# Kernel optimization log

Hardware: AMD Instinct MI355X
Metric: run time of the kernel (lower is better)

## Reference

```python
import jax, jax.numpy as jnp
import numpy as np

B, N1, N2 = 8, 16384, 2048
C1, C2 = 128, 256
IN_CH = C1 + C2  # 384
MLP = [256, 128]
BN_EPS = 1e-5


def setup_inputs() -> dict:
    key = jax.random.key(0)
    ks = jax.random.split(key, 12)
    inp = {
        "xyz1": jax.random.normal(ks[0], (B, N1, 3), dtype=jnp.float32),
        "xyz2": jax.random.normal(ks[1], (B, N2, 3), dtype=jnp.float32),
        "points1": jax.random.normal(ks[2], (B, N1, C1), dtype=jnp.float32),
        "points2": jax.random.normal(ks[3], (B, N2, C2), dtype=jnp.float32),
        # pointwise conv1d (kernel=1) weights as [out, in]
        "W1": jax.random.normal(ks[4], (MLP[0], IN_CH), dtype=jnp.float32) * (1.0 / np.sqrt(IN_CH)),
        "b1": jnp.zeros((MLP[0],), dtype=jnp.float32),
        "gamma1": jnp.ones((MLP[0],), dtype=jnp.float32),
        "beta1": jnp.zeros((MLP[0],), dtype=jnp.float32),
        "W2": jax.random.normal(ks[5], (MLP[1], MLP[0]), dtype=jnp.float32) * (1.0 / np.sqrt(MLP[0])),
        "b2": jnp.zeros((MLP[1],), dtype=jnp.float32),
        "gamma2": jnp.ones((MLP[1],), dtype=jnp.float32),
        "beta2": jnp.zeros((MLP[1],), dtype=jnp.float32),
    }
    return inp


def _bn_relu(h, gamma, beta):
    # BatchNorm1d in training mode: batch stats over (B, N) per channel
    mean = jnp.mean(h, axis=(0, 1), keepdims=True)
    var = jnp.mean((h - mean) ** 2, axis=(0, 1), keepdims=True)
    return jax.nn.relu((h - mean) * jax.lax.rsqrt(var + BN_EPS) * gamma + beta)


def reference(xyz1, xyz2, points1, points2, W1, b1, gamma1, beta1, W2, b2, gamma2, beta2):
    # squared pairwise distances [B, N1, N2]
    d = (-2.0 * jnp.einsum("bnc,bmc->bnm", xyz1, xyz2)
         + jnp.sum(xyz1 ** 2, -1)[:, :, None]
         + jnp.sum(xyz2 ** 2, -1)[:, None, :])
    neg_vals, idx = jax.lax.top_k(-d, 3)            # 3 smallest distances
    dists = jnp.maximum(-neg_vals, 1e-10)           # clamp(min=1e-10)
    w = 1.0 / dists                                 # [B, N1, 3]
    w_norm = w / jnp.maximum(jnp.sum(w, axis=2, keepdims=True), 1e-8)
    # gather 3 neighbor features: [B, N1, 3, C2]
    gathered = jax.vmap(lambda p, i: p[i])(points2, idx)
    interp = jnp.einsum("bnk,bnkc->bnc", w_norm, gathered)  # [B, N1, C2]
    x = jnp.concatenate([points1, interp], axis=-1)          # [B, N1, IN_CH]
    # pointwise conv + BN + ReLU stack
    h = jnp.einsum("bnc,oc->bno", x, W1) + b1
    h = _bn_relu(h, gamma1, beta1)
    h = jnp.einsum("bnc,oc->bno", h, W2) + b2
    h = _bn_relu(h, gamma2, beta2)
    return h  # [B, N1, MLP[-1]]
```

## Files before the change

### kernel.cpp

```cpp
#include <hip/hip_runtime.h>
#include <hip/hip_bf16.h>
#include <stdint.h>
#include <stddef.h>

typedef __hip_bfloat16 bf16;
typedef __attribute__((ext_vector_type(8))) short short8;
typedef __attribute__((ext_vector_type(4))) float f32x4;

#define B_SZ   8
#define N1_SZ  16384
#define N2_SZ  2048
#define C1_SZ  128
#define C2_SZ  256
#define IN_CH  384
#define O1_SZ  256
#define O2_SZ  128
#define R_TOT  (B_SZ * N1_SZ)

#define OFF_FLAG   ((size_t)0)
#define OFF_STATS1 ((size_t)256)
#define OFF_SCALE1 ((size_t)2304)
#define OFF_STATS2 ((size_t)4352)
#define OFF_SCALE2 ((size_t)5376)
#define OFF_WIDX   ((size_t)8192)
#define OFF_WW     ((size_t)1581056)
#define OFF_H1     ((size_t)3153920)
#define WS_NEEDED  ((size_t)70262784)


static __device__ __forceinline__ float cvtf(bf16 v) { return __bfloat162float(v); }
static __device__ __forceinline__ float cvtf(float v) { return v; }
static __device__ __forceinline__ bf16  f2b(float v) { return __float2bfloat16(v); }

static __device__ __forceinline__ void load8f(const bf16* p, float* f) {
  uint4 v = *(const uint4*)p;
  const bf16* e = (const bf16*)&v;
#pragma unroll
  for (int j = 0; j < 8; ++j) f[j] = cvtf(e[j]);
}
static __device__ __forceinline__ void load8f(const float* p, float* f) {
  float4 a = *(const float4*)p;
  float4 b = *(const float4*)(p + 4);
  f[0] = a.x; f[1] = a.y; f[2] = a.z; f[3] = a.w;
  f[4] = b.x; f[5] = b.y; f[6] = b.z; f[7] = b.w;
}
static __device__ __forceinline__ void load8b(const bf16* p, bf16* o) {
  *(uint4*)o = *(const uint4*)p;
}
static __device__ __forceinline__ void load8b(const float* p, bf16* o) {
  float f[8]; load8f(p, f);
#pragma unroll
  for (int j = 0; j < 8; ++j) o[j] = f2b(f[j]);
}
static __device__ __forceinline__ void stv(bf16* p, float v) { *p = f2b(v); }
static __device__ __forceinline__ void stv(float* p, float v) { *p = v; }
static __device__ __forceinline__ void store8(bf16* p, const bf16* t) { *(uint4*)p = *(const uint4*)t; }
static __device__ __forceinline__ void store8(float* p, const float* t) {
  *(uint4*)p = *(const uint4*)t; *(uint4*)(p + 4) = *(const uint4*)(t + 4);
}

__global__ void k_detect(const uint16_t* __restrict__ probe, int* __restrict__ flag) {
  __shared__ int cnt;
  if (threadIdx.x == 0) cnt = 0;
  __syncthreads();
  unsigned u = probe[threadIdx.x];
  int e = (u >> 7) & 0xFF;
  if (e >= 100 && e <= 141) atomicAdd(&cnt, 1);
  __syncthreads();
  if (threadIdx.x == 0) *flag = (cnt >= 224) ? 1 : 0;
}

template <typename T>
__global__ __launch_bounds__(256) void k_fill2(T* __restrict__ out,
                                               const int* __restrict__ flag, int expect) {
  if (flag && *flag != expect) return;
  size_t e0 = ((size_t)blockIdx.x * 256 + threadIdx.x) * 8;
  T t[8];
#pragma unroll
  for (int j = 0; j < 8; ++j) stv(&t[j], 2.0f);
  store8(out + e0, t);
}

static __device__ __forceinline__ void merge3(double& a0, double& a1, double& a2,
                                              int& x0, int& x1, int& x2, int mask) {
  double b0 = __shfl_xor(a0, mask, 64);
  double b1 = __shfl_xor(a1, mask, 64);
  double b2 = __shfl_xor(a2, mask, 64);
  int y0 = __shfl_xor(x0, mask, 64);
  int y1 = __shfl_xor(x1, mask, 64);
  int y2 = __shfl_xor(x2, mask, 64);
  bool t = (a0 < b0) || (a0 == b0 && x0 < y0);
  double c0 = t ? a0 : b0; int k0 = t ? x0 : y0;
  double A0 = t ? a1 : a0; int X0 = t ? x1 : x0;
  double A1 = t ? a2 : a1; int X1 = t ? x2 : x1;
  double B0 = t ? b0 : b1; int Y0 = t ? y0 : y1;
  double B1 = t ? b1 : b2; int Y1 = t ? y1 : y2;
  t = (A0 < B0) || (A0 == B0 && X0 < Y0);
  double c1 = t ? A0 : B0; int k1 = t ? X0 : Y0;
  double A0b = t ? A1 : A0; int X0b = t ? X1 : X0;
  double B0b = t ? B0 : B1; int Y0b = t ? Y0 : Y1;
  t = (A0b < B0b) || (A0b == B0b && X0b < Y0b);
  double c2 = t ? A0b : B0b; int k2 = t ? X0b : Y0b;
  a0 = c0; a1 = c1; a2 = c2; x0 = k0; x1 = k1; x2 = k2;
}

template <typename T>
__global__ __launch_bounds__(512) void k_top3(const T* __restrict__ xyz1,
                                              const T* __restrict__ xyz2,
                                              int* __restrict__ widx,
                                              float* __restrict__ ww,
                                              const int* __restrict__ flag, int expect) {
  if (*flag != expect) return;
  __shared__ float4 sp[N2_SZ];
  int b = blockIdx.x >> 7;
  int g = blockIdx.x & 127;
  const T* x2 = xyz2 + (size_t)b * N2_SZ * 3;
  for (int i = threadIdx.x; i < N2_SZ; i += 512) {
    float px = cvtf(x2[i * 3 + 0]);
    float py = cvtf(x2[i * 3 + 1]);
    float pz = cvtf(x2[i * 3 + 2]);
    double dx = (double)px, dy = (double)py, dz = (double)pz;
    float pw = (float)(dx * dx + dy * dy + dz * dz);
    sp[i] = make_float4(-2.f * px, -2.f * py, -2.f * pz, pw);
  }
  __syncthreads();
  int qloc = threadIdx.x >> 2;
  int sub  = threadIdx.x & 3;
  int n = g * 128 + qloc;
  int r = b * N1_SZ + n;
  float Qxf = cvtf(xyz1[(size_t)r * 3 + 0]);
  float Qyf = cvtf(xyz1[(size_t)r * 3 + 1]);
  float Qzf = cvtf(xyz1[(size_t)r * 3 + 2]);

  float m0 = 3.0e38f, m1 = 3.0e38f, m2 = 3.0e38f, m3 = 3.0e38f;
  int i0 = 0, i1 = 0, i2 = 0, i3 = 0;
#pragma unroll 4
  for (int i = 0; i < N2_SZ / 4; ++i) {
    int j = (i << 2) | sub;
    float4 p = sp[j];
    float d = fmaf(p.x, Qxf, fmaf(p.y, Qyf, fmaf(p.z, Qzf, p.w)));
    bool c0 = d < m0, c1 = d < m1, c2 = d < m2, c3 = d < m3;
    int t3 = c2 ? i2 : (c3 ? j : i3);
    int t2 = c1 ? i1 : (c2 ? j : i2);
    int t1 = c0 ? i0 : (c1 ? j : i1);
    int t0 = c0 ? j : i0;
    float v3 = __builtin_amdgcn_fmed3f(m2, m3, d);
    float v2 = __builtin_amdgcn_fmed3f(m1, m2, d);
    float v1 = __builtin_amdgcn_fmed3f(m0, m1, d);
    float v0 = fminf(m0, d);
    m0 = v0; m1 = v1; m2 = v2; m3 = v3;
    i0 = t0; i1 = t1; i2 = t2; i3 = t3;
  }

  double Qx = (double)Qxf, Qy = (double)Qyf, Qz = (double)Qzf;
  double Qn = Qx * Qx + Qy * Qy + Qz * Qz;
  double e0 = 1e300, e1 = 1e300, e2 = 1e300;
  int j0 = 0, j1 = 0, j2 = 0;
  int ys[4] = { i0, i1, i2, i3 };
#pragma unroll
  for (int k = 0; k < 4; ++k) {
    int j = ys[k];
    float4 p = sp[j];
    double Px = -0.5 * (double)p.x;
    double Py = -0.5 * (double)p.y;
    double Pz = -0.5 * (double)p.z;
    double pw = Px * Px + Py * Py + Pz * Pz;
    double dot = Qx * Px + Qy * Py + Qz * Pz;
    double d = fma(-2.0, dot, Qn + pw);
    bool l2 = (d < e2) || (d == e2 && j < j2);
    if (l2) {
      bool l1 = (d < e1) || (d == e1 && j < j1);
      if (l1) {
        e2 = e1; j2 = j1;
        bool l0 = (d < e0) || (d == e0 && j < j0);
        if (l0) { e1 = e0; j1 = j0; e0 = d; j0 = j; }
        else    { e1 = d;  j1 = j; }
      } else { e2 = d; j2 = j; }
    }
  }

  merge3(e0, e1, e2, j0, j1, j2, 1);
  merge3(e0, e1, e2, j0, j1, j2, 2);

  if (sub == 0) {
    e0 = fmax(e0, 1e-10); e1 = fmax(e1, 1e-10); e2 = fmax(e2, 1e-10);
    double w0 = 1.0 / e0, w1 = 1.0 / e1, w2 = 1.0 / e2;
    double inv = 1.0 / fmax(w0 + w1 + w2, 1e-8);
    widx[(size_t)r * 3 + 0] = j0; widx[(size_t)r * 3 + 1] = j1; widx[(size_t)r * 3 + 2] = j2;
    ww[(size_t)r * 3 + 0] = (float)(w0 * inv);
    ww[(size_t)r * 3 + 1] = (float)(w1 * inv);
    ww[(size_t)r * 3 + 2] = (float)(w2 * inv);
  }
}

template <typename T>
__global__ __launch_bounds__(256) void k_gemm1(const T* __restrict__ points1,
                                               const T* __restrict__ points2,
                                               const int* __restrict__ widx,
                                               const float* __restrict__ ww,
                                               const T* __restrict__ W1,
                                               const T* __restrict__ bias,
                                               bf16* __restrict__ h1,
                                               float* __restrict__ part,
                                               const int* __restrict__ flag, int expect) {
  if (*flag != expect) return;
  constexpr int LDA = 392;
  constexpr int LDT = 40;
  __shared__ bf16 As[64 * LDA];
  __shared__ bf16 Bs[256 * LDT];
  __shared__ float redu[2][256][2];

  int tid = threadIdx.x;
  int r0 = blockIdx.x * 64;
  int row = tid >> 2;
  int sub = tid & 3;
  int r = r0 + row;
  int bidx = r >> 14;
  int i0 = widx[(size_t)r * 3 + 0];
  int i1 = widx[(size_t)r * 3 + 1];
  int i2 = widx[(size_t)r * 3 + 2];
  float w0 = ww[(size_t)r * 3 + 0];
  float w1 = ww[(size_t)r * 3 + 1];
  float w2 = ww[(size_t)r * 3 + 2];
  const T* p2 = points2 + (size_t)bidx * N2_SZ * C2_SZ;

#pragma unroll
  for (int q = 0; q < 4; ++q) {
    int c = sub * 32 + q * 8;
    bf16 t[8];
    load8b(points1 + (size_t)r * C1_SZ + c, t);
    *(uint4*)&As[row * LDA + c] = *(uint4*)t;
  }
#pragma unroll 4
  for (int q = 0; q < 8; ++q) {
    int c = sub * 64 + q * 8;
    float f0[8], f1[8], f2[8];
    load8f(p2 + (size_t)i0 * C2_SZ + c, f0);
    load8f(p2 + (size_t)i1 * C2_SZ + c, f1);
    load8f(p2 + (size_t)i2 * C2_SZ + c, f2);
    bf16 t[8];
#pragma unroll
    for (int j = 0; j < 8; ++j)
      t[j] = f2b(w0 * f0[j] + w1 * f1[j] + w2 * f2[j]);
    *(uint4*)&As[row * LDA + C1_SZ + c] = *(uint4*)t;
  }
#pragma unroll
  for (int s = 0; s < 4; ++s) {
    int u = tid + s * 256;
    int orow = u >> 2, okc = (u & 3) * 8;
    bf16 wv0[8];
    load8b(W1 + (size_t)orow * IN_CH + okc, wv0);
    *(uint4*)&Bs[orow * LDT + okc] = *(uint4*)wv0;
  }

  int wave = tid >> 6, lane = tid & 63;
  int quad = lane >> 4, l15 = lane & 15;
  int wy = wave >> 1, wx = wave & 1;

  f32x4 acc[2][8];
#pragma unroll
  for (int tm = 0; tm < 2; ++tm)
#pragma unroll
    for (int tn = 0; tn < 8; ++tn) {
      acc[tm][tn][0] = 0.f; acc[tm][tn][1] = 0.f;
      acc[tm][tn][2] = 0.f; acc[tm][tn][3] = 0.f;
    }

  __syncthreads();

  for (int kk = 0; kk < 12; ++kk) {
    bf16 wv[4][8];
    if (kk < 11) {
#pragma unroll
      for (int s = 0; s < 4; ++s) {
        int u = tid + s * 256;
        int orow = u >> 2, okc = (u & 3) * 8;
        load8b(W1 + (size_t)orow * IN_CH + (kk + 1) * 32 + okc, wv[s]);
      }
    }
    short8 afr[2], bfr[8];
#pragma unroll
    for (int tm = 0; tm < 2; ++tm)
      afr[tm] = *(const short8*)&As[(wy * 32 + tm * 16 + l15) * LDA + kk * 32 + quad * 8];
#pragma unroll
    for (int tn = 0; tn < 8; ++tn)
      bfr[tn] = *(const short8*)&Bs[(wx * 128 + tn * 16 + l15) * LDT + quad * 8];
#pragma unroll
    for (int tm = 0; tm < 2; ++tm)
#pragma unroll
      for (int tn = 0; tn < 8; ++tn)
        acc[tm][tn] = __builtin_amdgcn_mfma_f32_16x16x32_bf16(afr[tm], bfr[tn], acc[tm][tn], 0, 0, 0);
    __syncthreads();
    if (kk < 11) {
#pragma unroll
      for (int s = 0; s < 4; ++s) {
        int u = tid + s * 256;
        int orow = u >> 2, okc = (u & 3) * 8;
        *(uint4*)&Bs[orow * LDT + okc] = *(uint4*)wv[s];
      }
      __syncthreads();
    }
  }

  float s1[8], s2[8];
#pragma unroll
  for (int tn = 0; tn < 8; ++tn) {
    int col = wx * 128 + tn * 16 + l15;
    float bv = cvtf(bias[col]);
    s1[tn] = 0.f; s2[tn] = 0.f;
#pragma unroll
    for (int tm = 0; tm < 2; ++tm) {
#pragma unroll
      for (int rg = 0; rg < 4; ++rg) {
        int rw = r0 + wy * 32 + tm * 16 + quad * 4 + rg;
        float vv = acc[tm][tn][rg] + bv;
        s1[tn] += vv; s2[tn] += vv * vv;
        h1[(size_t)rw * O1_SZ + col] = f2b(vv);
      }
    }
    s1[tn] += __shfl_xor(s1[tn], 16, 64);
    s1[tn] += __shfl_xor(s1[tn], 32, 64);
    s2[tn] += __shfl_xor(s2[tn], 16, 64);
    s2[tn] += __shfl_xor(s2[tn], 32, 64);
  }
  if (lane < 16) {
#pragma unroll
    for (int tn = 0; tn < 8; ++tn) {
      int col = wx * 128 + tn * 16 + l15;
      redu[wy][col][0] = s1[tn];
      redu[wy][col][1] = s2[tn];
    }
  }
  __syncthreads();
  {
    float* pb = part + (size_t)blockIdx.x * 512;
    pb[tid * 2 + 0] = redu[0][tid][0] + redu[1][tid][0];
    pb[tid * 2 + 1] = redu[0][tid][1] + redu[1][tid][1];
  }
}

template <typename T>
__global__ __launch_bounds__(256) void k_gemm2(const bf16* __restrict__ h1,
                                               const T* __restrict__ W2,
                                               const T* __restrict__ bias,
                                               const float* __restrict__ scale1,
                                               const float* __restrict__ shift1,
                                               T* __restrict__ out,
                                               float* __restrict__ part,
                                               const int* __restrict__ flag, int expect) {
  if (*flag != expect) return;
  constexpr int LDT = 40;
  __shared__ bf16 As[64 * LDT];
  __shared__ bf16 Bs[128 * LDT];
  __shared__ float redu[2][128][2];
  __shared__ float sc_s[O1_SZ], sh_s[O1_SZ];

  int tid = threadIdx.x;
  sc_s[tid] = scale1[tid];
  sh_s[tid] = shift1[tid];

  int r0 = blockIdx.x * 64;
  int arow = tid >> 2;
  int akc  = (tid & 3) * 8;

  int wave = tid >> 6, lane = tid & 63;
  int quad = lane >> 4, l15 = lane & 15;
  int wy = wave >> 1, wx = wave & 1;

  f32x4 acc[2][4];
#pragma unroll
  for (int tm = 0; tm < 2; ++tm)
#pragma unroll
    for (int tn = 0; tn < 4; ++tn) {
      acc[tm][tn][0] = 0.f; acc[tm][tn][1] = 0.f;
      acc[tm][tn][2] = 0.f; acc[tm][tn][3] = 0.f;
    }

  for (int k0 = 0; k0 < O1_SZ; k0 += 32) {
    __syncthreads();
    {
      uint4 v = *(const uint4*)(h1 + (size_t)(r0 + arow) * O1_SZ + k0 + akc);
      const bf16* e = (const bf16*)&v;
      bf16 t[8];
#pragma unroll
      for (int j = 0; j < 8; ++j) {
        float f = cvtf(e[j]);
        f = fmaxf(fmaf(f, sc_s[k0 + akc + j], sh_s[k0 + akc + j]), 0.f);
        t[j] = f2b(f);
      }
      *(uint4*)&As[arow * LDT + akc] = *(uint4*)t;
    }
#pragma unroll
    for (int s = 0; s < 2; ++s) {
      int u = tid + s * 256;
      int orow = u >> 2, okc = (u & 3) * 8;
      bf16 wv[8];
      load8b(W2 + (size_t)orow * O1_SZ + k0 + okc, wv);
      *(uint4*)&Bs[orow * LDT + okc] = *(uint4*)wv;
    }
    __syncthreads();
    short8 afr[2], bfr[4];
#pragma unroll
    for (int tm = 0; tm < 2; ++tm)
      afr[tm] = *(const short8*)&As[(wy * 32 + tm * 16 + l15) * LDT + quad * 8];
#pragma unroll
    for (int tn = 0; tn < 4; ++tn)
      bfr[tn] = *(const short8*)&Bs[(wx * 64 + tn * 16 + l15) * LDT + quad * 8];
#pragma unroll
    for (int tm = 0; tm < 2; ++tm)
#pragma unroll
      for (int tn = 0; tn < 4; ++tn)
        acc[tm][tn] = __builtin_amdgcn_mfma_f32_16x16x32_bf16(afr[tm], bfr[tn], acc[tm][tn], 0, 0, 0);
  }

  float s1[4], s2[4];
#pragma unroll
  for (int tn = 0; tn < 4; ++tn) {
    int col = wx * 64 + tn * 16 + l15;
    float bv = cvtf(bias[col]);
    s1[tn] = 0.f; s2[tn] = 0.f;
#pragma unroll
    for (int tm = 0; tm < 2; ++tm) {
#pragma unroll
      for (int rg = 0; rg < 4; ++rg) {
        int row = r0 + wy * 32 + tm * 16 + quad * 4 + rg;
        float vv = acc[tm][tn][rg] + bv;
        s1[tn] += vv; s2[tn] += vv * vv;
        stv(&out[(size_t)row * O2_SZ + col], vv);
      }
    }
    s1[tn] += __shfl_xor(s1[tn], 16, 64);
    s1[tn] += __shfl_xor(s1[tn], 32, 64);
    s2[tn] += __shfl_xor(s2[tn], 16, 64);
    s2[tn] += __shfl_xor(s2[tn], 32, 64);
  }
  if (lane < 16) {
#pragma unroll
    for (int tn = 0; tn < 4; ++tn) {
      int col = wx * 64 + tn * 16 + l15;
      redu[wy][col][0] = s1[tn];
      redu[wy][col][1] = s2[tn];
    }
  }
  __syncthreads();
  {
    int col = tid & 127;
    int sel = tid >> 7;
    part[(size_t)blockIdx.x * 256 + col * 2 + sel] = redu[0][col][sel] + redu[1][col][sel];
  }
}

__global__ __launch_bounds__(256) void k_reduce(const float* __restrict__ part,
                                                float* __restrict__ stats,
                                                int nblk, int nvals) {
  int v = blockIdx.x;
  float s = 0.f;
  for (int b = threadIdx.x; b < nblk; b += 256)
    s += part[(size_t)b * nvals + v];
  s += __shfl_xor(s, 1, 64);  s += __shfl_xor(s, 2, 64);
  s += __shfl_xor(s, 4, 64);  s += __shfl_xor(s, 8, 64);
  s += __shfl_xor(s, 16, 64); s += __shfl_xor(s, 32, 64);
  __shared__ float red[4];
  if ((threadIdx.x & 63) == 0) red[threadIdx.x >> 6] = s;
  __syncthreads();
  if (threadIdx.x == 0) stats[v] = red[0] + red[1] + red[2] + red[3];
}

template <typename T>
__global__ void k_bn_fin(const float* __restrict__ stats, const T* __restrict__ gamma,
                         const T* __restrict__ beta, float* __restrict__ scale,
                         float* __restrict__ shift, int O, float invR,
                         const int* __restrict__ flag, int expect) {
  if (*flag != expect) return;
  int t = blockIdx.x * blockDim.x + threadIdx.x;
  if (t < O) {
    float m = stats[t * 2 + 0] * invR;
    float var = fmaxf(stats[t * 2 + 1] * invR - m * m, 0.f);
    float is = rsqrtf(var + 1e-5f);
    float sc = cvtf(gamma[t]) * is;
    scale[t] = sc;
    shift[t] = cvtf(beta[t]) - m * sc;
  }
}

template <typename T>
__global__ __launch_bounds__(256) void k_bn_out(T* __restrict__ out,
                                                const float* __restrict__ scale,
                                                const float* __restrict__ shift,
                                                const int* __restrict__ flag, int expect) {
  if (*flag != expect) return;
  size_t e0 = ((size_t)blockIdx.x * 256 + threadIdx.x) * 8;
  int c0 = (int)(e0 & (O2_SZ - 1));
  float f[8]; load8f(out + e0, f);
  T t[8];
#pragma unroll
  for (int j = 0; j < 8; ++j) {
    float pre = fmaf(f[j], scale[c0 + j], shift[c0 + j]);
    float r = fmaxf(pre, 0.f);
    if (__builtin_isnan(pre)) r = pre;
    stv(&t[j], r);
  }
  store8(out + e0, t);
}

extern "C" void kernel_launch(void* const* d_in, const int* in_sizes, int n_in,
                              void* d_out, int out_size, void* d_ws, size_t ws_size,
                              hipStream_t stream) {
  char* ws = (char*)d_ws;
  int*   flag   = (int*)(ws + OFF_FLAG);
  float* stats1 = (float*)(ws + OFF_STATS1);
  float* scale1 = (float*)(ws + OFF_SCALE1);
  float* shift1 = scale1 + 256;
  float* stats2 = (float*)(ws + OFF_STATS2);
  float* scale2 = (float*)(ws + OFF_SCALE2);
  float* shift2 = scale2 + 128;
  int*   widx   = (int*)(ws + OFF_WIDX);
  float* wwp    = (float*)(ws + OFF_WW);
  bf16*  h1     = (bf16*)(ws + OFF_H1);
  float* part1  = (float*)d_out;
  float* part2  = (float*)(ws + OFF_WIDX);

  const int FILL_GRID = R_TOT * O2_SZ / 2048;

  if (ws_size < WS_NEEDED) {
    if (ws_size >= 256) {
      k_detect<<<1, 256, 0, stream>>>((const uint16_t*)d_in[2], flag);
      k_fill2<bf16><<<FILL_GRID, 256, 0, stream>>>((bf16*)d_out, flag, 1);
      k_fill2<float><<<FILL_GRID, 256, 0, stream>>>((float*)d_out, flag, 0);
    } else {
      k_fill2<bf16><<<FILL_GRID, 256, 0, stream>>>((bf16*)d_out, (const int*)nullptr, 0);
    }
    return;
  }

  k_detect<<<1, 256, 0, stream>>>((const uint16_t*)d_in[2], flag);

  float invR = 1.f / (float)R_TOT;

  k_top3<bf16><<<1024, 512, 0, stream>>>((const bf16*)d_in[0], (const bf16*)d_in[1], widx, wwp, flag, 1);
  k_top3<float><<<1024, 512, 0, stream>>>((const float*)d_in[0], (const float*)d_in[1], widx, wwp, flag, 0);

  k_gemm1<bf16><<<R_TOT / 64, 256, 0, stream>>>((const bf16*)d_in[2], (const bf16*)d_in[3],
      widx, wwp, (const bf16*)d_in[4], (const bf16*)d_in[5], h1, part1, flag, 1);
  k_gemm1<float><<<R_TOT / 64, 256, 0, stream>>>((const float*)d_in[2], (const float*)d_in[3],
      widx, wwp, (const float*)d_in[4], (const float*)d_in[5], h1, part1, flag, 0);

  k_reduce<<<512, 256, 0, stream>>>(part1, stats1, R_TOT / 64, 512);

  k_bn_fin<bf16><<<1, 256, 0, stream>>>(stats1, (const bf16*)d_in[6], (const bf16*)d_in[7],
      scale1, shift1, O1_SZ, invR, flag, 1);
  k_bn_fin<float><<<1, 256, 0, stream>>>(stats1, (const float*)d_in[6], (const float*)d_in[7],
      scale1, shift1, O1_SZ, invR, flag, 0);

  k_gemm2<bf16><<<R_TOT / 64, 256, 0, stream>>>(h1, (const bf16*)d_in[8], (const bf16*)d_in[9],
      scale1, shift1, (bf16*)d_out, part2, flag, 1);
  k_gemm2<float><<<R_TOT / 64, 256, 0, stream>>>(h1, (const float*)d_in[8], (const float*)d_in[9],
      scale1, shift1, (float*)d_out, part2, flag, 0);

  k_reduce<<<256, 256, 0, stream>>>(part2, stats2, R_TOT / 64, 256);

  k_bn_fin<bf16><<<1, 128, 0, stream>>>(stats2, (const bf16*)d_in[10], (const bf16*)d_in[11],
      scale2, shift2, O2_SZ, invR, flag, 1);
  k_bn_fin<float><<<1, 128, 0, stream>>>(stats2, (const float*)d_in[10], (const float*)d_in[11],
      scale2, shift2, O2_SZ, invR, flag, 0);

  k_bn_out<bf16><<<FILL_GRID, 256, 0, stream>>>((bf16*)d_out, scale2, shift2, flag, 1);
  k_bn_out<float><<<FILL_GRID, 256, 0, stream>>>((float*)d_out, scale2, shift2, flag, 0);
}
```

Measured before the change: 460.1 us.

## Pre-convert weights to bf16 and load MFMA B fragments directly from global

Adds a small kernel that converts W1 and W2 to bf16 scratch buffers once per call. The GEMMs then read B fragments straight from global or L2 instead of staging weight tiles through LDS with per-k-step barriers. gemm2 now stages the whole BN+ReLU-applied h1 tile into LDS once rather than per k-chunk, and the reduction scratch reuses the A tile buffer. This removes many syncthreads and LDS traffic, but relies on cache hits for the repeated global weight reads and adds two extra launches.

```diff
diff --git a/kernel.cpp b/kernel.cpp
--- a/kernel.cpp
+++ b/kernel.cpp
@@ -27,6 +27,8 @@
 #define OFF_H1     ((size_t)3153920)
 #define WS_NEEDED  ((size_t)70262784)
 
+#define W1B_DOUT_OFF ((size_t)8388608)
+#define W2B_WS_OFF   ((size_t)(8192 + 2621440))
 
 static __device__ __forceinline__ float cvtf(bf16 v) { return __bfloat162float(v); }
 static __device__ __forceinline__ float cvtf(float v) { return v; }
@@ -68,6 +70,19 @@
   if (e >= 100 && e <= 141) atomicAdd(&cnt, 1);
   __syncthreads();
   if (threadIdx.x == 0) *flag = (cnt >= 224) ? 1 : 0;
+}
+
+template <typename T>
+__global__ __launch_bounds__(256) void k_cvtw(const T* __restrict__ src,
+                                              bf16* __restrict__ dst, int n,
+                                              const int* __restrict__ flag, int expect) {
+  if (*flag != expect) return;
+  int i = ((int)blockIdx.x * 256 + threadIdx.x) * 8;
+  if (i < n) {
+    bf16 t[8];
+    load8b(src + i, t);
+    *(uint4*)&dst[i] = *(uint4*)t;
+  }
 }
 
 template <typename T>
@@ -198,17 +213,14 @@
                                                const T* __restrict__ points2,
                                                const int* __restrict__ widx,
                                                const float* __restrict__ ww,
-                                               const T* __restrict__ W1,
+                                               const bf16* __restrict__ W1b,
                                                const T* __restrict__ bias,
                                                bf16* __restrict__ h1,
                                                float* __restrict__ part,
                                                const int* __restrict__ flag, int expect) {
   if (*flag != expect) return;
   constexpr int LDA = 392;
-  constexpr int LDT = 40;
   __shared__ bf16 As[64 * LDA];
-  __shared__ bf16 Bs[256 * LDT];
-  __shared__ float redu[2][256][2];
 
   int tid = threadIdx.x;
   int r0 = blockIdx.x * 64;
@@ -244,14 +256,6 @@
       t[j] = f2b(w0 * f0[j] + w1 * f1[j] + w2 * f2[j]);
     *(uint4*)&As[row * LDA + C1_SZ + c] = *(uint4*)t;
   }
-#pragma unroll
-  for (int s = 0; s < 4; ++s) {
-    int u = tid + s * 256;
-    int orow = u >> 2, okc = (u & 3) * 8;
-    bf16 wv0[8];
-    load8b(W1 + (size_t)orow * IN_CH + okc, wv0);
-    *(uint4*)&Bs[orow * LDT + okc] = *(uint4*)wv0;
-  }
 
   int wave = tid >> 6, lane = tid & 63;
   int quad = lane >> 4, l15 = lane & 15;
@@ -266,41 +270,27 @@
       acc[tm][tn][2] = 0.f; acc[tm][tn][3] = 0.f;
     }
 
+  const bf16* wb = W1b + (size_t)(wx * 128 + l15) * IN_CH + quad * 8;
+
   __syncthreads();
 
   for (int kk = 0; kk < 12; ++kk) {
-    bf16 wv[4][8];
-    if (kk < 11) {
-#pragma unroll
-      for (int s = 0; s < 4; ++s) {
-        int u = tid + s * 256;
-        int orow = u >> 2, okc = (u & 3) * 8;
-        load8b(W1 + (size_t)orow * IN_CH + (kk + 1) * 32 + okc, wv[s]);
-      }
-    }
     short8 afr[2], bfr[8];
+#pragma unroll
+    for (int tn = 0; tn < 8; ++tn)
+      bfr[tn] = *(const short8*)(wb + (size_t)tn * 16 * IN_CH + kk * 32);
 #pragma unroll
     for (int tm = 0; tm < 2; ++tm)
       afr[tm] = *(const short8*)&As[(wy * 32 + tm * 16 + l15) * LDA + kk * 32 + quad * 8];
 #pragma unroll
-    for (int tn = 0; tn < 8; ++tn)
-      bfr[tn] = *(const short8*)&Bs[(wx * 128 + tn * 16 + l15) * LDT + quad * 8];
-#pragma unroll
     for (int tm = 0; tm < 2; ++tm)
 #pragma unroll
       for (int tn = 0; tn < 8; ++tn)
         acc[tm][tn] = __builtin_amdgcn_mfma_f32_16x16x32_bf16(afr[tm], bfr[tn], acc[tm][tn], 0, 0, 0);
-    __syncthreads();
-    if (kk < 11) {
-#pragma unroll
-      for (int s = 0; s < 4; ++s) {
-        int u = tid + s * 256;
-        int orow = u >> 2, okc = (u & 3) * 8;
-        *(uint4*)&Bs[orow * LDT + okc] = *(uint4*)wv[s];
-      }
-      __syncthreads();
-    }
-  }
+  }
+
+  __syncthreads();
+  float* redu = (float*)As;
 
   float s1[8], s2[8];
 #pragma unroll
@@ -327,21 +317,21 @@
 #pragma unroll
     for (int tn = 0; tn < 8; ++tn) {
       int col = wx * 128 + tn * 16 + l15;
-      redu[wy][col][0] = s1[tn];
-      redu[wy][col][1] = s2[tn];
+      redu[(wy * 256 + col) * 2 + 0] = s1[tn];
+      redu[(wy * 256 + col) * 2 + 1] = s2[tn];
     }
   }
   __syncthreads();
   {
     float* pb = part + (size_t)blockIdx.x * 512;
-    pb[tid * 2 + 0] = redu[0][tid][0] + redu[1][tid][0];
-    pb[tid * 2 + 1] = redu[0][tid][1] + redu[1][tid][1];
+    pb[tid * 2 + 0] = redu[tid * 2 + 0] + redu[(256 + tid) * 2 + 0];
+    pb[tid * 2 + 1] = redu[tid * 2 + 1] + redu[(256 + tid) * 2 + 1];
   }
 }
 
 template <typename T>
 __global__ __launch_bounds__(256) void k_gemm2(const bf16* __restrict__ h1,
-                                               const T* __restrict__ W2,
+                                               const bf16* __restrict__ W2b,
                                                const T* __restrict__ bias,
                                                const float* __restrict__ scale1,
                                                const float* __restrict__ shift1,
@@ -349,19 +339,35 @@
                                                float* __restrict__ part,
                                                const int* __restrict__ flag, int expect) {
   if (*flag != expect) return;
-  constexpr int LDT = 40;
-  __shared__ bf16 As[64 * LDT];
-  __shared__ bf16 Bs[128 * LDT];
-  __shared__ float redu[2][128][2];
+  constexpr int LDK = 264;
+  __shared__ bf16 As[64 * LDK];
   __shared__ float sc_s[O1_SZ], sh_s[O1_SZ];
 
   int tid = threadIdx.x;
   sc_s[tid] = scale1[tid];
   sh_s[tid] = shift1[tid];
+  __syncthreads();
 
   int r0 = blockIdx.x * 64;
-  int arow = tid >> 2;
-  int akc  = (tid & 3) * 8;
+  int row = tid >> 2;
+  int seg = tid & 3;
+  {
+    const bf16* hrow = h1 + (size_t)(r0 + row) * O1_SZ + seg * 64;
+#pragma unroll
+    for (int q = 0; q < 8; ++q) {
+      int c = seg * 64 + q * 8;
+      uint4 v = *(const uint4*)(hrow + q * 8);
+      const bf16* e = (const bf16*)&v;
+      bf16 t[8];
+#pragma unroll
+      for (int j = 0; j < 8; ++j) {
+        float f = cvtf(e[j]);
+        f = fmaxf(fmaf(f, sc_s[c + j], sh_s[c + j]), 0.f);
+        t[j] = f2b(f);
+      }
+      *(uint4*)&As[row * LDK + c] = *(uint4*)t;
+    }
+  }
 
   int wave = tid >> 6, lane = tid & 63;
   int quad = lane >> 4, l15 = lane & 15;
@@ -376,42 +382,27 @@
       acc[tm][tn][2] = 0.f; acc[tm][tn][3] = 0.f;
     }
 
-  for (int k0 = 0; k0 < O1_SZ; k0 += 32) {
-    __syncthreads();
-    {
-      uint4 v = *(const uint4*)(h1 + (size_t)(r0 + arow) * O1_SZ + k0 + akc);
-      const bf16* e = (const bf16*)&v;
-      bf16 t[8];
-#pragma unroll
-      for (int j = 0; j < 8; ++j) {
-        float f = cvtf(e[j]);
-        f = fmaxf(fmaf(f, sc_s[k0 + akc + j], sh_s[k0 + akc + j]), 0.f);
-        t[j] = f2b(f);
-      }
-      *(uint4*)&As[arow * LDT + akc] = *(uint4*)t;
-    }
-#pragma unroll
-    for (int s = 0; s < 2; ++s) {
-      int u = tid + s * 256;
-      int orow = u >> 2, okc = (u & 3) * 8;
-      bf16 wv[8];
-      load8b(W2 + (size_t)orow * O1_SZ + k0 + okc, wv);
-      *(uint4*)&Bs[orow * LDT + okc] = *(uint4*)wv;
-    }
-    __syncthreads();
+  const bf16* wb = W2b + (size_t)(wx * 64 + l15) * O1_SZ + quad * 8;
+
+  __syncthreads();
+
+  for (int kk = 0; kk < 8; ++kk) {
     short8 afr[2], bfr[4];
 #pragma unroll
+    for (int tn = 0; tn < 4; ++tn)
+      bfr[tn] = *(const short8*)(wb + (size_t)tn * 16 * O1_SZ + kk * 32);
+#pragma unroll
     for (int tm = 0; tm < 2; ++tm)
-      afr[tm] = *(const short8*)&As[(wy * 32 + tm * 16 + l15) * LDT + quad * 8];
-#pragma unroll
-    for (int tn = 0; tn < 4; ++tn)
-      bfr[tn] = *(const short8*)&Bs[(wx * 64 + tn * 16 + l15) * LDT + quad * 8];
+      afr[tm] = *(const short8*)&As[(wy * 32 + tm * 16 + l15) * LDK + kk * 32 + quad * 8];
 #pragma unroll
     for (int tm = 0; tm < 2; ++tm)
 #pragma unroll
       for (int tn = 0; tn < 4; ++tn)
         acc[tm][tn] = __builtin_amdgcn_mfma_f32_16x16x32_bf16(afr[tm], bfr[tn], acc[tm][tn], 0, 0, 0);
   }
+
+  __syncthreads();
+  float* redu = (float*)As;
 
   float s1[4], s2[4];
 #pragma unroll
@@ -423,10 +414,10 @@
     for (int tm = 0; tm < 2; ++tm) {
 #pragma unroll
       for (int rg = 0; rg < 4; ++rg) {
-        int row = r0 + wy * 32 + tm * 16 + quad * 4 + rg;
+        int rw = r0 + wy * 32 + tm * 16 + quad * 4 + rg;
         float vv = acc[tm][tn][rg] + bv;
         s1[tn] += vv; s2[tn] += vv * vv;
-        stv(&out[(size_t)row * O2_SZ + col], vv);
+        stv(&out[(size_t)rw * O2_SZ + col], vv);
       }
     }
     s1[tn] += __shfl_xor(s1[tn], 16, 64);
@@ -438,15 +429,16 @@
 #pragma unroll
     for (int tn = 0; tn < 4; ++tn) {
       int col = wx * 64 + tn * 16 + l15;
-      redu[wy][col][0] = s1[tn];
-      redu[wy][col][1] = s2[tn];
+      redu[(wy * 128 + col) * 2 + 0] = s1[tn];
+      redu[(wy * 128 + col) * 2 + 1] = s2[tn];
     }
   }
   __syncthreads();
   {
     int col = tid & 127;
     int sel = tid >> 7;
-    part[(size_t)blockIdx.x * 256 + col * 2 + sel] = redu[0][col][sel] + redu[1][col][sel];
+    part[(size_t)blockIdx.x * 256 + col * 2 + sel] =
+        redu[col * 2 + sel] + redu[(128 + col) * 2 + sel];
   }
 }
 
@@ -519,6 +511,8 @@
   bf16*  h1     = (bf16*)(ws + OFF_H1);
   float* part1  = (float*)d_out;
   float* part2  = (float*)(ws + OFF_WIDX);
+  bf16*  W1b    = (bf16*)((char*)d_out + W1B_DOUT_OFF);
+  bf16*  W2b    = (bf16*)(ws + W2B_WS_OFF);
 
   const int FILL_GRID = R_TOT * O2_SZ / 2048;
 
@@ -537,13 +531,19 @@
 
   float invR = 1.f / (float)R_TOT;
 
+  k_cvtw<bf16><<<48, 256, 0, stream>>>((const bf16*)d_in[4], W1b, IN_CH * O1_SZ, flag, 1);
+  k_cvtw<float><<<48, 256, 0, stream>>>((const float*)d_in[4], W1b, IN_CH * O1_SZ, flag, 0);
+
   k_top3<bf16><<<1024, 512, 0, stream>>>((const bf16*)d_in[0], (const bf16*)d_in[1], widx, wwp, flag, 1);
   k_top3<float><<<1024, 512, 0, stream>>>((const float*)d_in[0], (const float*)d_in[1], widx, wwp, flag, 0);
 
   k_gemm1<bf16><<<R_TOT / 64, 256, 0, stream>>>((const bf16*)d_in[2], (const bf16*)d_in[3],
-      widx, wwp, (const bf16*)d_in[4], (const bf16*)d_in[5], h1, part1, flag, 1);
+      widx, wwp, W1b, (const bf16*)d_in[5], h1, part1, flag, 1);
   k_gemm1<float><<<R_TOT / 64, 256, 0, stream>>>((const float*)d_in[2], (const float*)d_in[3],
-      widx, wwp, (const float*)d_in[4], (const float*)d_in[5], h1, part1, flag, 0);
+      widx, wwp, W1b, (const float*)d_in[5], h1, part1, flag, 0);
+
+  k_cvtw<bf16><<<16, 256, 0, stream>>>((const bf16*)d_in[8], W2b, O1_SZ * O2_SZ, flag, 1);
+  k_cvtw<float><<<16, 256, 0, stream>>>((const float*)d_in[8], W2b, O1_SZ * O2_SZ, flag, 0);
 
   k_reduce<<<512, 256, 0, stream>>>(part1, stats1, R_TOT / 64, 512);
 
@@ -552,9 +552,9 @@
   k_bn_fin<float><<<1, 256, 0, stream>>>(stats1, (const float*)d_in[6], (const float*)d_in[7],
       scale1, shift1, O1_SZ, invR, flag, 0);
 
-  k_gemm2<bf16><<<R_TOT / 64, 256, 0, stream>>>(h1, (const bf16*)d_in[8], (const bf16*)d_in[9],
+  k_gemm2<bf16><<<R_TOT / 64, 256, 0, stream>>>(h1, W2b, (const bf16*)d_in[9],
       scale1, shift1, (bf16*)d_out, part2, flag, 1);
-  k_gemm2<float><<<R_TOT / 64, 256, 0, stream>>>(h1, (const float*)d_in[8], (const float*)d_in[9],
+  k_gemm2<float><<<R_TOT / 64, 256, 0, stream>>>(h1, W2b, (const float*)d_in[9],
       scale1, shift1, (float*)d_out, part2, flag, 0);
 
   k_reduce<<<256, 256, 0, stream>>>(part2, stats2, R_TOT / 64, 256);
```

Measured after the change: 525.8 us. 14.3% more time.
